# Kernel optimization log

Measured on AMD Instinct MI355X. Metric: run time of the kernel, lower is better.

Reference implementation:

```python
import jax, jax.numpy as jnp
import numpy as np

D = 512       # model_dim
H = 8         # num_heads
DH = D // H   # dim_per_head
LN_EPS = 1e-5


def setup_inputs() -> dict:
    key = jax.random.key(0)
    ks = jax.random.split(key, 10)
    B, S = 2, 2048
    s = D ** -0.5
    return {
        "query": jax.random.normal(ks[0], (B, S, D), jnp.float32),
        "key":   jax.random.normal(ks[1], (B, S, D), jnp.float32),
        "value": jax.random.normal(ks[2], (B, S, D), jnp.float32),
        # torch Linear weights: [out, in], y = x @ W.T
        "Wq": jax.random.normal(ks[3], (D, D), jnp.float32) * s,
        "Wk": jax.random.normal(ks[4], (D, D), jnp.float32) * s,
        "Wv": jax.random.normal(ks[5], (D, D), jnp.float32) * s,
        "Wo": jax.random.normal(ks[6], (D, D), jnp.float32) * s,
        "bo": jnp.zeros((D,), jnp.float32),
        "gamma": jnp.ones((D,), jnp.float32),
        "beta":  jnp.zeros((D,), jnp.float32),
    }


def _layer_norm(x, gamma, beta):
    mu = jnp.mean(x, axis=-1, keepdims=True)
    var = jnp.var(x, axis=-1, keepdims=True)
    return (x - mu) * jax.lax.rsqrt(var + LN_EPS) * gamma + beta


def reference(query, key, value, Wq, Wk, Wv, Wo, bo, gamma, beta):
    B, S, _ = query.shape
    residual = query
    # projections (torch Linear: x @ W.T), split heads -> [B, H, S, DH]
    q = (query @ Wq.T).reshape(B, S, H, DH).transpose(0, 2, 1, 3)
    k = (key   @ Wk.T).reshape(B, S, H, DH).transpose(0, 2, 1, 3)
    v = (value @ Wv.T).reshape(B, S, H, DH).transpose(0, 2, 1, 3)
    scale = DH ** -0.5
    scores = jnp.einsum('bhqd,bhkd->bhqk', q, k) * scale
    attention = jax.nn.softmax(scores, axis=-1)
    context = jnp.einsum('bhqk,bhkd->bhqd', attention, v)
    context = context.transpose(0, 2, 1, 3).reshape(B, S, D)
    output = context @ Wo.T + bo
    output = _layer_norm(residual + output, gamma, beta)
    # original returns attention as [B*H, S, S]
    return output, attention.reshape(B * H, S, S)
```

## Files before the change

### kernel.cpp

```cpp
#include <hip/hip_runtime.h>

#define B_ 2
#define S_ 2048
#define D_ 512
#define H_ 8
#define DH_ 64

typedef __bf16 bf16_8 __attribute__((ext_vector_type(8)));
typedef float f32x4 __attribute__((ext_vector_type(4)));
typedef unsigned int u32x4 __attribute__((ext_vector_type(4)));

union BfPack4 { ushort4 u; __bf16 h[4]; };

__global__ __launch_bounds__(256) void proj_qkv(
    const float* __restrict__ Xq, const float* __restrict__ Xk, const float* __restrict__ Xv,
    const float* __restrict__ Wq, const float* __restrict__ Wk, const float* __restrict__ Wv,
    __bf16* __restrict__ Qb, __bf16* __restrict__ Kb, __bf16* __restrict__ Vt)
{
    const int z = blockIdx.z;
    const float* X = (z == 0) ? Xq : (z == 1) ? Xk : Xv;
    const float* W = (z == 0) ? Wq : (z == 1) ? Wk : Wv;
    const int m0 = blockIdx.x * 64;
    const int n0 = blockIdx.y * 64;

    __shared__ __bf16 Xs[64][72];
    __shared__ __bf16 Ws[64][72];

    const int tid = threadIdx.x;
    const int w = tid >> 6, lane = tid & 63;
    const int quad = lane >> 4, mc = lane & 15;

    int rr[4], cc[4];
    for (int i = 0; i < 4; ++i) { int e = tid + i * 256; rr[i] = e >> 4; cc[i] = (e & 15) * 4; }

    f32x4 acc[4] = {};
    float4 xr[4], wv[4];
    for (int i = 0; i < 4; ++i) {
        xr[i] = *reinterpret_cast<const float4*>(&X[(size_t)(m0 + rr[i]) * 512 + cc[i]]);
        wv[i] = *reinterpret_cast<const float4*>(&W[(size_t)(n0 + rr[i]) * 512 + cc[i]]);
    }

    for (int kc = 0; kc < 512; kc += 64) {
        if (kc) __syncthreads();
        for (int i = 0; i < 4; ++i) {
            BfPack4 px, pw;
            px.h[0] = (__bf16)xr[i].x; px.h[1] = (__bf16)xr[i].y;
            px.h[2] = (__bf16)xr[i].z; px.h[3] = (__bf16)xr[i].w;
            *reinterpret_cast<ushort4*>(&Xs[rr[i]][cc[i]]) = px.u;
            pw.h[0] = (__bf16)wv[i].x; pw.h[1] = (__bf16)wv[i].y;
            pw.h[2] = (__bf16)wv[i].z; pw.h[3] = (__bf16)wv[i].w;
            *reinterpret_cast<ushort4*>(&Ws[rr[i]][cc[i]]) = pw.u;
        }
        __syncthreads();
        if (kc < 448) {
            for (int i = 0; i < 4; ++i) {
                xr[i] = *reinterpret_cast<const float4*>(&X[(size_t)(m0 + rr[i]) * 512 + kc + 64 + cc[i]]);
                wv[i] = *reinterpret_cast<const float4*>(&W[(size_t)(n0 + rr[i]) * 512 + kc + 64 + cc[i]]);
            }
        }
        for (int ks = 0; ks < 64; ks += 32) {
            bf16_8 a = *reinterpret_cast<const bf16_8*>(&Xs[w * 16 + mc][ks + quad * 8]);
            for (int tt = 0; tt < 4; ++tt) {
                bf16_8 bb = *reinterpret_cast<const bf16_8*>(&Ws[tt * 16 + mc][ks + quad * 8]);
                acc[tt] = __builtin_amdgcn_mfma_f32_16x16x32_bf16(a, bb, acc[tt], 0, 0, 0);
            }
        }
    }
    __syncthreads();
    const float scale = (z == 0) ? 0.125f : 1.0f;
    if (z < 2) {
        for (int tt = 0; tt < 4; ++tt)
            for (int r = 0; r < 4; ++r)
                Xs[w * 16 + quad * 4 + r][tt * 16 + mc] = (__bf16)(acc[tt][r] * scale);
    } else {
        for (int tt = 0; tt < 4; ++tt)
            for (int r = 0; r < 4; ++r)
                Xs[tt * 16 + mc][w * 16 + quad * 4 + r] = (__bf16)acc[tt][r];
    }
    __syncthreads();
    if (z < 2) {
        __bf16* out = (z == 0) ? Qb : Kb;
        for (int i = 0; i < 2; ++i) {
            int e = tid + i * 256;
            int r = e >> 3, c8 = (e & 7) * 8;
            *reinterpret_cast<uint4*>(&out[(size_t)(m0 + r) * 512 + n0 + c8]) =
                *reinterpret_cast<const uint4*>(&Xs[r][c8]);
        }
    } else {
        int b = m0 >> 11, s0 = m0 & 2047, h = n0 >> 6;
        for (int i = 0; i < 2; ++i) {
            int e = tid + i * 256;
            int r = e >> 3, c8 = (e & 7) * 8;
            *reinterpret_cast<uint4*>(&Vt[(((size_t)(b * H_ + h)) * DH_ + r) * S_ + s0 + c8]) =
                *reinterpret_cast<const uint4*>(&Xs[r][c8]);
        }
    }
}

__global__ __launch_bounds__(256) void attn_kernel(
    const __bf16* __restrict__ Qb, const __bf16* __restrict__ Kb, const __bf16* __restrict__ Vt,
    __bf16* __restrict__ Ctx, __bf16* __restrict__ Pws, float* __restrict__ Linv)
{
    const int qt = blockIdx.x;
    const int bh = blockIdx.y;
    const int b = bh >> 3, h = bh & 7;
    const int q0 = qt * 64;

    __shared__ __bf16 Qs[64][72];
    __shared__ __bf16 Ks[128][72];
    __shared__ __bf16 Ps[64][136];
    __shared__ __bf16 Vs[64][136];

    const int tid = threadIdx.x;
    const int w = tid >> 6, lane = tid & 63;
    const int quad = lane >> 4, mc = lane & 15;

    for (int i = 0; i < 2; ++i) {
        int e = tid + i * 256;
        int r = e >> 3, c8 = (e & 7) * 8;
        *reinterpret_cast<uint4*>(&Qs[r][c8]) =
            *reinterpret_cast<const uint4*>(&Qb[((size_t)b * S_ + q0 + r) * D_ + h * DH_ + c8]);
    }
    __syncthreads();
    const bf16_8 aq0 = *reinterpret_cast<const bf16_8*>(&Qs[w * 16 + mc][quad * 8]);
    const bf16_8 aq1 = *reinterpret_cast<const bf16_8*>(&Qs[w * 16 + mc][32 + quad * 8]);

    int kr[4], kcc[4], vr[4], vc[4];
    for (int i = 0; i < 4; ++i) {
        int e = tid + i * 256;
        kr[i] = e >> 3; kcc[i] = (e & 7) * 8;
        vr[i] = e >> 4; vc[i]  = (e & 15) * 8;
    }
    const __bf16* kp = Kb + (size_t)b * S_ * D_ + h * DH_;
    const __bf16* vp = Vt + (size_t)bh * DH_ * S_;

    uint4 kreg[4], vreg[4];
    for (int i = 0; i < 4; ++i) {
        kreg[i] = *reinterpret_cast<const uint4*>(&kp[(size_t)kr[i] * D_ + kcc[i]]);
        vreg[i] = *reinterpret_cast<const uint4*>(&vp[(size_t)vr[i] * S_ + vc[i]]);
    }

    float l[4] = {0.f, 0.f, 0.f, 0.f};
    f32x4 o[4] = {};

    for (int tc = 0; tc < 16; ++tc) {
        if (tc) __syncthreads();
        for (int i = 0; i < 4; ++i) {
            *reinterpret_cast<uint4*>(&Ks[kr[i]][kcc[i]]) = kreg[i];
            *reinterpret_cast<uint4*>(&Vs[vr[i]][vc[i]]) = vreg[i];
        }
        __syncthreads();
        if (tc < 15) {
            for (int i = 0; i < 4; ++i) {
                kreg[i] = *reinterpret_cast<const uint4*>(
                    &kp[(size_t)((tc + 1) * 128 + kr[i]) * D_ + kcc[i]]);
                vreg[i] = *reinterpret_cast<const uint4*>(
                    &vp[(size_t)vr[i] * S_ + (tc + 1) * 128 + vc[i]]);
            }
        }
        f32x4 s[8] = {};
        for (int ct = 0; ct < 8; ++ct) {
            bf16_8 b0 = *reinterpret_cast<const bf16_8*>(&Ks[ct * 16 + mc][quad * 8]);
            s[ct] = __builtin_amdgcn_mfma_f32_16x16x32_bf16(aq0, b0, s[ct], 0, 0, 0);
        }
        for (int ct = 0; ct < 8; ++ct) {
            bf16_8 b1 = *reinterpret_cast<const bf16_8*>(&Ks[ct * 16 + mc][32 + quad * 8]);
            s[ct] = __builtin_amdgcn_mfma_f32_16x16x32_bf16(aq1, b1, s[ct], 0, 0, 0);
        }
        for (int ct = 0; ct < 8; ++ct)
            for (int r = 0; r < 4; ++r) {
                float p = __expf(s[ct][r]);
                l[r] += p;
                Ps[w * 16 + quad * 4 + r][ct * 16 + mc] = (__bf16)p;
            }
        const int kc = tc * 128;
        for (int i = 0; i < 4; ++i) {
            int r = w * 16 + i * 4 + quad;
            u32x4 pu = *reinterpret_cast<const u32x4*>(&Ps[r][mc * 8]);
            __builtin_nontemporal_store(pu, reinterpret_cast<u32x4*>(
                &Pws[((size_t)bh * S_ + q0 + r) * S_ + kc + mc * 8]));
        }
        for (int ks = 0; ks < 128; ks += 32) {
            bf16_8 ap = *reinterpret_cast<const bf16_8*>(&Ps[w * 16 + mc][ks + quad * 8]);
            for (int tt = 0; tt < 4; ++tt) {
                bf16_8 bv = *reinterpret_cast<const bf16_8*>(&Vs[tt * 16 + mc][ks + quad * 8]);
                o[tt] = __builtin_amdgcn_mfma_f32_16x16x32_bf16(ap, bv, o[tt], 0, 0, 0);
            }
        }
    }
    for (int r = 0; r < 4; ++r)
        for (int off = 1; off < 16; off <<= 1) l[r] += __shfl_xor(l[r], off);
    float linv[4];
    for (int r = 0; r < 4; ++r) linv[r] = 1.f / l[r];
    if (mc == 0)
        for (int r = 0; r < 4; ++r)
            Linv[(size_t)bh * S_ + q0 + w * 16 + quad * 4 + r] = linv[r];

    __syncthreads();
    for (int tt = 0; tt < 4; ++tt)
        for (int r = 0; r < 4; ++r)
            Qs[w * 16 + quad * 4 + r][tt * 16 + mc] = (__bf16)(o[tt][r] * linv[r]);
    __syncthreads();
    for (int i = 0; i < 2; ++i) {
        int e = tid + i * 256;
        int r = e >> 3, c8 = (e & 7) * 8;
        *reinterpret_cast<uint4*>(&Ctx[((size_t)b * S_ + q0 + r) * D_ + h * DH_ + c8]) =
            *reinterpret_cast<const uint4*>(&Qs[r][c8]);
    }
}

__global__ __launch_bounds__(256) void rescale_kernel(
    const __bf16* __restrict__ Pws, const float* __restrict__ Linv,
    float* __restrict__ attn_out)
{
    const int row = blockIdx.x;
    const float s = Linv[row];
    const int c = threadIdx.x * 8;
    const size_t base = (size_t)row * S_ + c;
    u32x4 pu = __builtin_nontemporal_load(reinterpret_cast<const u32x4*>(&Pws[base]));
    const __bf16* p = reinterpret_cast<const __bf16*>(&pu);
    f32x4 lo, hi;
    for (int j = 0; j < 4; ++j) {
        lo[j] = (float)p[j] * s;
        hi[j] = (float)p[j + 4] * s;
    }
    float* dst = &attn_out[base];
    __builtin_nontemporal_store(lo, reinterpret_cast<f32x4*>(dst));
    __builtin_nontemporal_store(hi, reinterpret_cast<f32x4*>(dst + 4));
}

__global__ __launch_bounds__(256) void oproj(
    const __bf16* __restrict__ Ctx, const float* __restrict__ Wo,
    const float* __restrict__ bo, const float* __restrict__ resid,
    float* __restrict__ Y)
{
    const int m0 = blockIdx.x * 64;
    const int n0 = blockIdx.y * 64;

    __shared__ __bf16 As[64][72];
    __shared__ __bf16 Bs[64][72];

    const int tid = threadIdx.x;
    const int w = tid >> 6, lane = tid & 63;
    const int quad = lane >> 4, mc = lane & 15;

    int ar[2], ac[2], wr2[4], wc2[4];
    for (int i = 0; i < 2; ++i) { int e = tid + i * 256; ar[i] = e >> 3; ac[i] = (e & 7) * 8; }
    for (int i = 0; i < 4; ++i) { int e = tid + i * 256; wr2[i] = e >> 4; wc2[i] = (e & 15) * 4; }

    uint4 areg[2];
    float4 wreg[4];
    for (int i = 0; i < 2; ++i)
        areg[i] = *reinterpret_cast<const uint4*>(&Ctx[(size_t)(m0 + ar[i]) * 512 + ac[i]]);
    for (int i = 0; i < 4; ++i)
        wreg[i] = *reinterpret_cast<const float4*>(&Wo[(size_t)(n0 + wr2[i]) * 512 + wc2[i]]);

    f32x4 acc[4] = {};
    for (int kc = 0; kc < 512; kc += 64) {
        if (kc) __syncthreads();
        for (int i = 0; i < 2; ++i)
            *reinterpret_cast<uint4*>(&As[ar[i]][ac[i]]) = areg[i];
        for (int i = 0; i < 4; ++i) {
            BfPack4 pw;
            pw.h[0] = (__bf16)wreg[i].x; pw.h[1] = (__bf16)wreg[i].y;
            pw.h[2] = (__bf16)wreg[i].z; pw.h[3] = (__bf16)wreg[i].w;
            *reinterpret_cast<ushort4*>(&Bs[wr2[i]][wc2[i]]) = pw.u;
        }
        __syncthreads();
        if (kc < 448) {
            for (int i = 0; i < 2; ++i)
                areg[i] = *reinterpret_cast<const uint4*>(&Ctx[(size_t)(m0 + ar[i]) * 512 + kc + 64 + ac[i]]);
            for (int i = 0; i < 4; ++i)
                wreg[i] = *reinterpret_cast<const float4*>(&Wo[(size_t)(n0 + wr2[i]) * 512 + kc + 64 + wc2[i]]);
        }
        for (int ks = 0; ks < 64; ks += 32) {
            bf16_8 a = *reinterpret_cast<const bf16_8*>(&As[w * 16 + mc][ks + quad * 8]);
            for (int tt = 0; tt < 4; ++tt) {
                bf16_8 bb = *reinterpret_cast<const bf16_8*>(&Bs[tt * 16 + mc][ks + quad * 8]);
                acc[tt] = __builtin_amdgcn_mfma_f32_16x16x32_bf16(a, bb, acc[tt], 0, 0, 0);
            }
        }
    }
    for (int tt = 0; tt < 4; ++tt) {
        int col = n0 + tt * 16 + mc;
        float bias = bo[col];
        for (int r = 0; r < 4; ++r) {
            int row = m0 + w * 16 + quad * 4 + r;
            Y[(size_t)row * 512 + col] = acc[tt][r] + bias + resid[(size_t)row * 512 + col];
        }
    }
}

__global__ __launch_bounds__(256) void ln_kernel(
    const float* __restrict__ Y, const float* __restrict__ gamma,
    const float* __restrict__ beta, float* __restrict__ out)
{
    const int row = blockIdx.x * 4 + (threadIdx.x >> 6);
    const int lane = threadIdx.x & 63;
    const float* y = &Y[(size_t)row * 512];
    float4 v0 = *reinterpret_cast<const float4*>(&y[lane * 8]);
    float4 v1 = *reinterpret_cast<const float4*>(&y[lane * 8 + 4]);
    float sum = v0.x + v0.y + v0.z + v0.w + v1.x + v1.y + v1.z + v1.w;
    float sq = v0.x * v0.x + v0.y * v0.y + v0.z * v0.z + v0.w * v0.w +
               v1.x * v1.x + v1.y * v1.y + v1.z * v1.z + v1.w * v1.w;
    for (int off = 1; off < 64; off <<= 1) {
        sum += __shfl_xor(sum, off);
        sq  += __shfl_xor(sq, off);
    }
    const float mean = sum * (1.f / 512.f);
    const float var = sq * (1.f / 512.f) - mean * mean;
    const float rstd = rsqrtf(var + 1e-5f);
    float4 g0 = *reinterpret_cast<const float4*>(&gamma[lane * 8]);
    float4 g1 = *reinterpret_cast<const float4*>(&gamma[lane * 8 + 4]);
    float4 b0 = *reinterpret_cast<const float4*>(&beta[lane * 8]);
    float4 b1 = *reinterpret_cast<const float4*>(&beta[lane * 8 + 4]);
    float4 o0, o1;
    o0.x = (v0.x - mean) * rstd * g0.x + b0.x;
    o0.y = (v0.y - mean) * rstd * g0.y + b0.y;
    o0.z = (v0.z - mean) * rstd * g0.z + b0.z;
    o0.w = (v0.w - mean) * rstd * g0.w + b0.w;
    o1.x = (v1.x - mean) * rstd * g1.x + b1.x;
    o1.y = (v1.y - mean) * rstd * g1.y + b1.y;
    o1.z = (v1.z - mean) * rstd * g1.z + b1.z;
    o1.w = (v1.w - mean) * rstd * g1.w + b1.w;
    *reinterpret_cast<float4*>(&out[(size_t)row * 512 + lane * 8]) = o0;
    *reinterpret_cast<float4*>(&out[(size_t)row * 512 + lane * 8 + 4]) = o1;
}

extern "C" void kernel_launch(void* const* d_in, const int* in_sizes, int n_in,
                              void* d_out, int out_size, void* d_ws, size_t ws_size,
                              hipStream_t stream)
{
    const float* query = (const float*)d_in[0];
    const float* key   = (const float*)d_in[1];
    const float* value = (const float*)d_in[2];
    const float* Wq    = (const float*)d_in[3];
    const float* Wk    = (const float*)d_in[4];
    const float* Wv    = (const float*)d_in[5];
    const float* Wo    = (const float*)d_in[6];
    const float* bo    = (const float*)d_in[7];
    const float* gamma = (const float*)d_in[8];
    const float* beta  = (const float*)d_in[9];

    float* out = (float*)d_out;
    float* attn_out = out + (size_t)B_ * S_ * D_;

    char* ws = (char*)d_ws;
    __bf16* Qb  = (__bf16*)(ws);
    __bf16* Kb  = (__bf16*)(ws + (4u << 20));
    __bf16* Vt  = (__bf16*)(ws + (8u << 20));
    __bf16* Ctx = (__bf16*)(ws + (12u << 20));
    float*  Y   = (float*)(ws + (16u << 20));
    float*  Linv= (float*)(ws + (24u << 20));
    __bf16* Pws = (__bf16*)(ws + (32u << 20));

    proj_qkv<<<dim3(64, 8, 3), 256, 0, stream>>>(query, key, value, Wq, Wk, Wv, Qb, Kb, Vt);
    attn_kernel<<<dim3(32, 16), 256, 0, stream>>>(Qb, Kb, Vt, Ctx, Pws, Linv);
    rescale_kernel<<<B_ * H_ * S_, 256, 0, stream>>>(Pws, Linv, attn_out);
    oproj<<<dim3(64, 8), 256, 0, stream>>>(Ctx, Wo, bo, query, Y);
    ln_kernel<<<1024, 256, 0, stream>>>(Y, gamma, beta, out);
}
```

Before: 487.8 us.

## Fuse softmax normalization into attention kernel with split-K waves over 16-row query tiles

Removes the bf16 probability workspace and the separate rescale kernel. Each block now handles 16 query rows, and its four waves each cover a quarter of the keys, keeping the full unnormalized P row slice in LDS. After the row sums are combined across waves, the block writes the normalized fp32 attention directly and reduces the partial context outputs through shared memory. K and V are read straight from global memory instead of being staged in LDS, so K/V traffic per query rises four-fold. The trade is that redundant read, plus reduced LDS reuse, against eliminating a write and read of a 128 MB bf16 intermediate.

Measured after the change: 474.7 us. 1.03x faster.

```diff
diff --git a/kernel.cpp b/kernel.cpp
--- a/kernel.cpp
+++ b/kernel.cpp
@@ -99,134 +99,102 @@
 
 __global__ __launch_bounds__(256) void attn_kernel(
     const __bf16* __restrict__ Qb, const __bf16* __restrict__ Kb, const __bf16* __restrict__ Vt,
-    __bf16* __restrict__ Ctx, __bf16* __restrict__ Pws, float* __restrict__ Linv)
+    __bf16* __restrict__ Ctx, float* __restrict__ attn_out)
 {
     const int qt = blockIdx.x;
     const int bh = blockIdx.y;
     const int b = bh >> 3, h = bh & 7;
-    const int q0 = qt * 64;
-
-    __shared__ __bf16 Qs[64][72];
-    __shared__ __bf16 Ks[128][72];
-    __shared__ __bf16 Ps[64][136];
-    __shared__ __bf16 Vs[64][136];
+    const int q0 = qt * 16;
+
+    __shared__ __align__(16) char smem[4 * 16 * 528 * 2];
+    __shared__ float Lsh[4][16];
 
     const int tid = threadIdx.x;
-    const int w = tid >> 6, lane = tid & 63;
+    const int kg = tid >> 6, lane = tid & 63;
     const int quad = lane >> 4, mc = lane & 15;
 
-    for (int i = 0; i < 2; ++i) {
-        int e = tid + i * 256;
-        int r = e >> 3, c8 = (e & 7) * 8;
-        *reinterpret_cast<uint4*>(&Qs[r][c8]) =
-            *reinterpret_cast<const uint4*>(&Qb[((size_t)b * S_ + q0 + r) * D_ + h * DH_ + c8]);
-    }
-    __syncthreads();
-    const bf16_8 aq0 = *reinterpret_cast<const bf16_8*>(&Qs[w * 16 + mc][quad * 8]);
-    const bf16_8 aq1 = *reinterpret_cast<const bf16_8*>(&Qs[w * 16 + mc][32 + quad * 8]);
-
-    int kr[4], kcc[4], vr[4], vc[4];
-    for (int i = 0; i < 4; ++i) {
-        int e = tid + i * 256;
-        kr[i] = e >> 3; kcc[i] = (e & 7) * 8;
-        vr[i] = e >> 4; vc[i]  = (e & 15) * 8;
-    }
-    const __bf16* kp = Kb + (size_t)b * S_ * D_ + h * DH_;
-    const __bf16* vp = Vt + (size_t)bh * DH_ * S_;
-
-    uint4 kreg[4], vreg[4];
-    for (int i = 0; i < 4; ++i) {
-        kreg[i] = *reinterpret_cast<const uint4*>(&kp[(size_t)kr[i] * D_ + kcc[i]]);
-        vreg[i] = *reinterpret_cast<const uint4*>(&vp[(size_t)vr[i] * S_ + vc[i]]);
-    }
+    __bf16* PsW = reinterpret_cast<__bf16*>(smem) + (size_t)kg * 16 * 528;
+
+    const __bf16* qrow = &Qb[((size_t)b * S_ + q0 + mc) * D_ + h * DH_];
+    const bf16_8 aq0 = *reinterpret_cast<const bf16_8*>(&qrow[quad * 8]);
+    const bf16_8 aq1 = *reinterpret_cast<const bf16_8*>(&qrow[32 + quad * 8]);
+
+    const __bf16* kbase = Kb + ((size_t)b * S_ + kg * 512) * D_ + h * DH_;
+    const __bf16* vbase = Vt + (size_t)bh * DH_ * S_ + kg * 512;
 
     float l[4] = {0.f, 0.f, 0.f, 0.f};
     f32x4 o[4] = {};
 
-    for (int tc = 0; tc < 16; ++tc) {
-        if (tc) __syncthreads();
-        for (int i = 0; i < 4; ++i) {
-            *reinterpret_cast<uint4*>(&Ks[kr[i]][kcc[i]]) = kreg[i];
-            *reinterpret_cast<uint4*>(&Vs[vr[i]][vc[i]]) = vreg[i];
-        }
-        __syncthreads();
-        if (tc < 15) {
-            for (int i = 0; i < 4; ++i) {
-                kreg[i] = *reinterpret_cast<const uint4*>(
-                    &kp[(size_t)((tc + 1) * 128 + kr[i]) * D_ + kcc[i]]);
-                vreg[i] = *reinterpret_cast<const uint4*>(
-                    &vp[(size_t)vr[i] * S_ + (tc + 1) * 128 + vc[i]]);
+    for (int c = 0; c < 8; ++c) {
+        const __bf16* kc_ = kbase + (size_t)c * 64 * D_;
+        bf16_8 kb[8];
+        for (int tt = 0; tt < 4; ++tt)
+            kb[tt] = *reinterpret_cast<const bf16_8*>(&kc_[(size_t)(tt * 16 + mc) * D_ + quad * 8]);
+        for (int tt = 0; tt < 4; ++tt)
+            kb[4 + tt] = *reinterpret_cast<const bf16_8*>(&kc_[(size_t)(tt * 16 + mc) * D_ + 32 + quad * 8]);
+        f32x4 s[4] = {};
+        for (int tt = 0; tt < 4; ++tt)
+            s[tt] = __builtin_amdgcn_mfma_f32_16x16x32_bf16(aq0, kb[tt], s[tt], 0, 0, 0);
+        for (int tt = 0; tt < 4; ++tt)
+            s[tt] = __builtin_amdgcn_mfma_f32_16x16x32_bf16(aq1, kb[4 + tt], s[tt], 0, 0, 0);
+        for (int tt = 0; tt < 4; ++tt)
+            for (int j = 0; j < 4; ++j) {
+                float p = __expf(s[tt][j]);
+                l[j] += p;
+                PsW[(size_t)(quad * 4 + j) * 528 + c * 64 + tt * 16 + mc] = (__bf16)p;
             }
-        }
-        f32x4 s[8] = {};
-        for (int ct = 0; ct < 8; ++ct) {
-            bf16_8 b0 = *reinterpret_cast<const bf16_8*>(&Ks[ct * 16 + mc][quad * 8]);
-            s[ct] = __builtin_amdgcn_mfma_f32_16x16x32_bf16(aq0, b0, s[ct], 0, 0, 0);
-        }
-        for (int ct = 0; ct < 8; ++ct) {
-            bf16_8 b1 = *reinterpret_cast<const bf16_8*>(&Ks[ct * 16 + mc][32 + quad * 8]);
-            s[ct] = __builtin_amdgcn_mfma_f32_16x16x32_bf16(aq1, b1, s[ct], 0, 0, 0);
-        }
-        for (int ct = 0; ct < 8; ++ct)
-            for (int r = 0; r < 4; ++r) {
-                float p = __expf(s[ct][r]);
-                l[r] += p;
-                Ps[w * 16 + quad * 4 + r][ct * 16 + mc] = (__bf16)p;
-            }
-        const int kc = tc * 128;
-        for (int i = 0; i < 4; ++i) {
-            int r = w * 16 + i * 4 + quad;
-            u32x4 pu = *reinterpret_cast<const u32x4*>(&Ps[r][mc * 8]);
-            __builtin_nontemporal_store(pu, reinterpret_cast<u32x4*>(
-                &Pws[((size_t)bh * S_ + q0 + r) * S_ + kc + mc * 8]));
-        }
-        for (int ks = 0; ks < 128; ks += 32) {
-            bf16_8 ap = *reinterpret_cast<const bf16_8*>(&Ps[w * 16 + mc][ks + quad * 8]);
-            for (int tt = 0; tt < 4; ++tt) {
-                bf16_8 bv = *reinterpret_cast<const bf16_8*>(&Vs[tt * 16 + mc][ks + quad * 8]);
-                o[tt] = __builtin_amdgcn_mfma_f32_16x16x32_bf16(ap, bv, o[tt], 0, 0, 0);
-            }
-        }
-    }
-    for (int r = 0; r < 4; ++r)
-        for (int off = 1; off < 16; off <<= 1) l[r] += __shfl_xor(l[r], off);
-    float linv[4];
-    for (int r = 0; r < 4; ++r) linv[r] = 1.f / l[r];
+        bf16_8 vb[8];
+        for (int ks2 = 0; ks2 < 2; ++ks2)
+            for (int tt = 0; tt < 4; ++tt)
+                vb[ks2 * 4 + tt] = *reinterpret_cast<const bf16_8*>(
+                    &vbase[(size_t)(tt * 16 + mc) * S_ + c * 64 + ks2 * 32 + quad * 8]);
+        for (int ks2 = 0; ks2 < 2; ++ks2) {
+            bf16_8 ap = *reinterpret_cast<const bf16_8*>(&PsW[(size_t)mc * 528 + c * 64 + ks2 * 32 + quad * 8]);
+            for (int tt = 0; tt < 4; ++tt)
+                o[tt] = __builtin_amdgcn_mfma_f32_16x16x32_bf16(ap, vb[ks2 * 4 + tt], o[tt], 0, 0, 0);
+        }
+    }
+
+    for (int j = 0; j < 4; ++j)
+        for (int off = 1; off < 16; off <<= 1) l[j] += __shfl_xor(l[j], off);
     if (mc == 0)
-        for (int r = 0; r < 4; ++r)
-            Linv[(size_t)bh * S_ + q0 + w * 16 + quad * 4 + r] = linv[r];
-
-    __syncthreads();
+        for (int j = 0; j < 4; ++j) Lsh[kg][quad * 4 + j] = l[j];
+    __syncthreads();
+
+    for (int row = 0; row < 16; ++row) {
+        const float li = 1.f / (Lsh[0][row] + Lsh[1][row] + Lsh[2][row] + Lsh[3][row]);
+        u32x4 pv = *reinterpret_cast<const u32x4*>(&PsW[(size_t)row * 528 + lane * 8]);
+        const __bf16* pp = reinterpret_cast<const __bf16*>(&pv);
+        f32x4 lo, hi;
+        for (int j = 0; j < 4; ++j) {
+            lo[j] = (float)pp[j] * li;
+            hi[j] = (float)pp[j + 4] * li;
+        }
+        float* dst = &attn_out[((size_t)bh * S_ + q0 + row) * S_ + kg * 512 + lane * 8];
+        __builtin_nontemporal_store(lo, reinterpret_cast<f32x4*>(dst));
+        __builtin_nontemporal_store(hi, reinterpret_cast<f32x4*>(dst + 4));
+    }
+    __syncthreads();
+
+    float* Osc = reinterpret_cast<float*>(smem);
     for (int tt = 0; tt < 4; ++tt)
-        for (int r = 0; r < 4; ++r)
-            Qs[w * 16 + quad * 4 + r][tt * 16 + mc] = (__bf16)(o[tt][r] * linv[r]);
-    __syncthreads();
-    for (int i = 0; i < 2; ++i) {
-        int e = tid + i * 256;
-        int r = e >> 3, c8 = (e & 7) * 8;
-        *reinterpret_cast<uint4*>(&Ctx[((size_t)b * S_ + q0 + r) * D_ + h * DH_ + c8]) =
-            *reinterpret_cast<const uint4*>(&Qs[r][c8]);
-    }
-}
-
-__global__ __launch_bounds__(256) void rescale_kernel(
-    const __bf16* __restrict__ Pws, const float* __restrict__ Linv,
-    float* __restrict__ attn_out)
-{
-    const int row = blockIdx.x;
-    const float s = Linv[row];
-    const int c = threadIdx.x * 8;
-    const size_t base = (size_t)row * S_ + c;
-    u32x4 pu = __builtin_nontemporal_load(reinterpret_cast<const u32x4*>(&Pws[base]));
-    const __bf16* p = reinterpret_cast<const __bf16*>(&pu);
-    f32x4 lo, hi;
-    for (int j = 0; j < 4; ++j) {
-        lo[j] = (float)p[j] * s;
-        hi[j] = (float)p[j + 4] * s;
-    }
-    float* dst = &attn_out[base];
-    __builtin_nontemporal_store(lo, reinterpret_cast<f32x4*>(dst));
-    __builtin_nontemporal_store(hi, reinterpret_cast<f32x4*>(dst + 4));
+        for (int j = 0; j < 4; ++j)
+            Osc[(size_t)kg * 16 * 68 + (quad * 4 + j) * 68 + tt * 16 + mc] = o[tt][j];
+    __syncthreads();
+    {
+        const int row = tid >> 4;
+        const int dhg = (tid & 15) * 4;
+        const float li = 1.f / (Lsh[0][row] + Lsh[1][row] + Lsh[2][row] + Lsh[3][row]);
+        BfPack4 pk;
+        for (int kk = 0; kk < 4; ++kk) {
+            float v = Osc[(size_t)0 * 16 * 68 + row * 68 + dhg + kk]
+                    + Osc[(size_t)1 * 16 * 68 + row * 68 + dhg + kk]
+                    + Osc[(size_t)2 * 16 * 68 + row * 68 + dhg + kk]
+                    + Osc[(size_t)3 * 16 * 68 + row * 68 + dhg + kk];
+            pk.h[kk] = (__bf16)(v * li);
+        }
+        *reinterpret_cast<ushort4*>(&Ctx[((size_t)b * S_ + q0 + row) * D_ + h * DH_ + dhg]) = pk.u;
+    }
 }
 
 __global__ __launch_bounds__(256) void oproj(
@@ -351,12 +319,9 @@
     __bf16* Vt  = (__bf16*)(ws + (8u << 20));
     __bf16* Ctx = (__bf16*)(ws + (12u << 20));
     float*  Y   = (float*)(ws + (16u << 20));
-    float*  Linv= (float*)(ws + (24u << 20));
-    __bf16* Pws = (__bf16*)(ws + (32u << 20));
 
     proj_qkv<<<dim3(64, 8, 3), 256, 0, stream>>>(query, key, value, Wq, Wk, Wv, Qb, Kb, Vt);
-    attn_kernel<<<dim3(32, 16), 256, 0, stream>>>(Qb, Kb, Vt, Ctx, Pws, Linv);
-    rescale_kernel<<<B_ * H_ * S_, 256, 0, stream>>>(Pws, Linv, attn_out);
+    attn_kernel<<<dim3(128, 16), 256, 0, stream>>>(Qb, Kb, Vt, Ctx, attn_out);
     oproj<<<dim3(64, 8), 256, 0, stream>>>(Ctx, Wo, bo, query, Y);
     ln_kernel<<<1024, 256, 0, stream>>>(Y, gamma, beta, out);
 }
```
